# Kernel tuning notes

Measured on AMD Instinct MI355X. Metric: run time of the kernel, lower is better.

## Reference

```python
import jax, jax.numpy as jnp
import numpy as np

DILATIONS = (1, 2, 4, 8)
NUM_ITER = 10
W1 = 0.3
W2 = 0.01
# 3x3 neighborhood excluding center, row-major (matches get_kernel ordering)
OFFS = ((0, 0), (0, 1), (0, 2), (1, 0), (1, 2), (2, 0), (2, 1), (2, 2))
# distance weights: sqrt(2) for diagonals (indices 0,2,5,7), 1 otherwise
POS_VALS = np.array([np.sqrt(2), 1.0, np.sqrt(2), 1.0, 1.0, np.sqrt(2), 1.0, np.sqrt(2)], dtype=np.float32)


def dilated_neighbors(x):
    # x: [b, c, h, w] -> [b, c, K, h, w], K = 8 * len(DILATIONS)
    b, c, h, w = x.shape
    outs = []
    for d in DILATIONS:
        xp = jnp.pad(x, ((0, 0), (0, 0), (d, d), (d, d)), mode='edge')
        for di, dj in OFFS:
            outs.append(jax.lax.dynamic_slice(xp, (0, 0, di * d, dj * d), (b, c, h, w)))
    return jnp.stack(outs, axis=2)


def pos_vec():
    # [K] concatenation of POS_VALS * d for each dilation
    return jnp.concatenate([jnp.asarray(POS_VALS) * d for d in DILATIONS], axis=0)


def setup_inputs() -> dict:
    key = jax.random.key(0)
    k1, k2 = jax.random.split(key)
    imgs = jax.random.normal(k1, (8, 3, 128, 128), dtype=jnp.float32)
    masks = jax.random.uniform(k2, (8, 21, 128, 128), dtype=jnp.float32)
    return {"imgs": imgs, "masks": masks}


def reference(imgs, masks):
    # pixel affinity: [b, 1, K, h, w]
    nb = dilated_neighbors(imgs)                                  # [b,c,K,h,w]
    diff = jnp.abs(nb - imgs[:, :, None, :, :])
    std = jnp.std(nb, axis=2, ddof=1, keepdims=True)              # unbiased, like torch.std
    aff = -((diff / (std + 1e-8) / W1) ** 2).mean(axis=1, keepdims=True)

    # position affinity: constant over b,h,w -> compute on the [K] vector
    pos = pos_vec()                                               # [K]
    pos_std = jnp.std(pos, ddof=1)
    pos_aff = -((pos / (pos_std + 1e-8) / W1) ** 2)

    aff = jax.nn.softmax(aff, axis=2) + W2 * jax.nn.softmax(pos_aff)[None, None, :, None, None]

    for _ in range(NUM_ITER):
        masks = (dilated_neighbors(masks) * aff).sum(axis=2)
    return masks
```

## Files before the change

kernel.cpp:

```cpp
#include <hip/hip_runtime.h>
#include <cmath>

#define B_   8
#define CI_  3
#define CM_  21
#define H_   128
#define W_   128
#define K_   32
#define PAD_ 8
#define PW_  144
#define PH_  144
#define NC_  3

typedef float f4 __attribute__((ext_vector_type(4)));
typedef _Float16 h4 __attribute__((ext_vector_type(4)));
typedef _Float16 h8v __attribute__((ext_vector_type(8)));

struct PosSoft { float v[K_]; };

template<int S>
__device__ __forceinline__ h4 shwh(h4 A, h4 B) {
  return __builtin_shufflevector(A, B, S, S + 1, S + 2, S + 3);
}

__device__ __forceinline__ h4 lda(const _Float16* p, int off) {
  return *reinterpret_cast<const h4*>(p + off);
}

__global__ __launch_bounds__(128) void aff_kernel(const float* __restrict__ imgs,
                                                  _Float16* __restrict__ aff,
                                                  PosSoft ps) {
  constexpr int OI[8] = {-1,-1,-1, 0, 0, 1, 1, 1};
  constexpr int OJ[8] = {-1, 0, 1,-1, 1,-1, 0, 1};
  const int j = threadIdx.x;
  const int i = blockIdx.x;
  const int b = blockIdx.y;
  const float* img = imgs + (size_t)b * CI_ * H_ * W_;

  float ctr[CI_];
#pragma unroll
  for (int c = 0; c < CI_; ++c) ctr[c] = img[c * H_ * W_ + i * W_ + j];

  float s[CI_] = {0.f, 0.f, 0.f}, s2[CI_] = {0.f, 0.f, 0.f};
#pragma unroll
  for (int k = 0; k < K_; ++k) {
    const int d  = 1 << (k >> 3);
    const int ci = min(max(i + OI[k & 7] * d, 0), H_ - 1);
    const int cj = min(max(j + OJ[k & 7] * d, 0), W_ - 1);
#pragma unroll
    for (int c = 0; c < CI_; ++c) {
      float v = img[c * H_ * W_ + ci * W_ + cj];
      s[c] += v; s2[c] += v * v;
    }
  }

  float inv[CI_];
#pragma unroll
  for (int c = 0; c < CI_; ++c) {
    float mean = s[c] * (1.f / K_);
    float var  = (s2[c] - (float)K_ * mean * mean) * (1.f / (K_ - 1));
    var = fmaxf(var, 0.f);
    inv[c] = 1.f / ((sqrtf(var) + 1e-8f) * 0.3f);
  }

  float araw[K_];
#pragma unroll
  for (int k = 0; k < K_; ++k) {
    const int d  = 1 << (k >> 3);
    const int ci = min(max(i + OI[k & 7] * d, 0), H_ - 1);
    const int cj = min(max(j + OJ[k & 7] * d, 0), W_ - 1);
    float t = 0.f;
#pragma unroll
    for (int c = 0; c < CI_; ++c) {
      float v  = img[c * H_ * W_ + ci * W_ + cj];
      float dd = fabsf(v - ctr[c]) * inv[c];
      t += dd * dd;
    }
    araw[k] = -t * (1.f / CI_);
  }

  float m = araw[0];
#pragma unroll
  for (int k = 1; k < K_; ++k) m = fmaxf(m, araw[k]);
  float sum = 0.f;
#pragma unroll
  for (int k = 0; k < K_; ++k) { float e = __expf(araw[k] - m); araw[k] = e; sum += e; }
  const float rs = 1.f / sum;

  _Float16* ap = aff + ((size_t)(b * H_ + i) * K_) * W_ + j;
#pragma unroll
  for (int k = 0; k < K_; ++k) ap[k * W_] = (_Float16)(araw[k] * rs + ps.v[k]);
}

__global__ void pad_kernel(const float* __restrict__ src, _Float16* __restrict__ dst,
                           int total4) {
  int idx = blockIdx.x * blockDim.x + threadIdx.x;
  if (idx >= total4) return;
  int q  = idx % (PW_ / 4);
  int t  = idx / (PW_ / 4);
  int pi = t % PH_;
  int p  = t / PH_;
  int i = min(max(pi - PAD_, 0), H_ - 1);
  const float* srow = src + (size_t)p * (H_ * W_) + i * W_;
  h4 o;
#pragma unroll
  for (int e = 0; e < 4; ++e) {
    int j = min(max(q * 4 + e - PAD_, 0), W_ - 1);
    o[e] = (_Float16)srow[j];
  }
  *reinterpret_cast<h4*>(dst + (size_t)p * (PH_ * PW_) + pi * PW_ + q * 4) = o;
}

#define LX(C, DR, CO) (lb + ((C) * 2880 + ((DR) + 8) * 144 + ((CO) + 8)))
#define LDSH(IDX) (*reinterpret_cast<const h4*>(&sm[(IDX)]))

#define HCH(C, ACC) do {                                                       \
    h4 m2 = LDSH(LX(C, 0, -8)), m1 = LDSH(LX(C, 0, -4));                       \
    h4 c0 = LDSH(LX(C, 0, 0)),  c1 = LDSH(LX(C, 0, 4));                        \
    h4 c2 = LDSH(LX(C, 0, 8));                                                 \
    ACC += a03 * shwh<3>(m1, c0) + a04 * shwh<1>(c0, c1);                      \
    ACC += a13 * shwh<2>(m1, c0) + a14 * shwh<2>(c0, c1);                      \
    ACC += a23 * m1 + a24 * c1;                                                \
    ACC += a33 * m2 + a34 * c2;                                                \
  } while (0)

#define VCHS(D, SM, A0, A1, A2, A5, A6, A7, C, ACC) do {                       \
    h4 ua = LDSH(LX(C, -(D), -4)), ub = LDSH(LX(C, -(D), 0));                  \
    h4 uc = LDSH(LX(C, -(D), 4));                                              \
    ACC += A0 * shwh<SM>(ua, ub) + A1 * ub + A2 * shwh<D>(ub, uc);             \
    h4 da = LDSH(LX(C, (D), -4)), db = LDSH(LX(C, (D), 0));                    \
    h4 dc = LDSH(LX(C, (D), 4));                                               \
    ACC += A5 * shwh<SM>(da, db) + A6 * db + A7 * shwh<D>(db, dc);             \
  } while (0)

#define VCH4(A0, A1, A2, A5, A6, A7, C, ACC) do {                              \
    h4 ua = LDSH(LX(C, -4, -4)), ub = LDSH(LX(C, -4, 0)), uc = LDSH(LX(C, -4, 4)); \
    ACC += A0 * ua + A1 * ub + A2 * uc;                                        \
    h4 da = LDSH(LX(C, 4, -4)), db = LDSH(LX(C, 4, 0)), dc = LDSH(LX(C, 4, 4)); \
    ACC += A5 * da + A6 * db + A7 * dc;                                        \
  } while (0)

#define VCH8(A0, A1, A2, A5, A6, A7, C, ACC) do {                              \
    h4 ua = LDSH(LX(C, -8, -8)), ub = LDSH(LX(C, -8, 0)), uc = LDSH(LX(C, -8, 8)); \
    ACC += A0 * ua + A1 * ub + A2 * uc;                                        \
    h4 da = LDSH(LX(C, 8, -8)), db = LDSH(LX(C, 8, 0)), dc = LDSH(LX(C, 8, 8)); \
    ACC += A5 * da + A6 * db + A7 * dc;                                        \
  } while (0)

template <int PADOUT>
__global__ __launch_bounds__(128, 3) void iter_kernel(const _Float16* __restrict__ src,
                                                      const _Float16* __restrict__ aff,
                                                      void* __restrict__ dstv) {
  __shared__ _Float16 sm[NC_ * 20 * PW_];

  const int bid  = blockIdx.x;
  const int b    = bid & 7;
  const int t    = bid >> 3;
  const int grp  = t % 7;
  const int tile = t / 7;

  const int tid = threadIdx.x;
  const int qx  = tid & 31;
  const int j0  = qx * 4;
  const int tr  = tid >> 5;
  const int i   = tile * 4 + tr;
  const int i0  = tile * 4;
  const int c0  = grp * NC_;

  constexpr int CHP = PH_ * PW_;

  const _Float16* ab = aff + ((size_t)(b * H_ + i) * K_) * W_ + j0;
  h4 a00 = lda(ab,  0 * W_), a01 = lda(ab,  1 * W_), a02 = lda(ab,  2 * W_),
     a03 = lda(ab,  3 * W_), a04 = lda(ab,  4 * W_), a05 = lda(ab,  5 * W_),
     a06 = lda(ab,  6 * W_), a07 = lda(ab,  7 * W_);
  h4 a10 = lda(ab,  8 * W_), a11 = lda(ab,  9 * W_), a12 = lda(ab, 10 * W_),
     a13 = lda(ab, 11 * W_), a14 = lda(ab, 12 * W_), a15 = lda(ab, 13 * W_),
     a16 = lda(ab, 14 * W_), a17 = lda(ab, 15 * W_);
  h4 a20 = lda(ab, 16 * W_), a21 = lda(ab, 17 * W_), a22 = lda(ab, 18 * W_),
     a23 = lda(ab, 19 * W_), a24 = lda(ab, 20 * W_), a25 = lda(ab, 21 * W_),
     a26 = lda(ab, 22 * W_), a27 = lda(ab, 23 * W_);
  h4 a30 = lda(ab, 24 * W_), a31 = lda(ab, 25 * W_), a32 = lda(ab, 26 * W_),
     a33 = lda(ab, 27 * W_), a34 = lda(ab, 28 * W_), a35 = lda(ab, 29 * W_),
     a36 = lda(ab, 30 * W_), a37 = lda(ab, 31 * W_);

  {
    const _Float16* pl = src + (size_t)(b * CM_ + c0) * CHP + (size_t)i0 * PW_;
    for (int s = tid; s < 1080; s += 128) {
      int c = s / 360;
      int r = s - c * 360;
      h8v v = *reinterpret_cast<const h8v*>(pl + (size_t)c * CHP + r * 8);
      *reinterpret_cast<h8v*>(&sm[c * 2880 + r * 8]) = v;
    }
  }
  __syncthreads();

  const int lb = tr * PW_ + j0;

  h4 acc0 = (h4){0, 0, 0, 0};
  h4 acc1 = (h4){0, 0, 0, 0};
  h4 acc2 = (h4){0, 0, 0, 0};

  HCH(0, acc0); HCH(1, acc1); HCH(2, acc2);

  VCHS(1, 3, a00, a01, a02, a05, a06, a07, 0, acc0);
  VCHS(1, 3, a00, a01, a02, a05, a06, a07, 1, acc1);
  VCHS(1, 3, a00, a01, a02, a05, a06, a07, 2, acc2);

  VCHS(2, 2, a10, a11, a12, a15, a16, a17, 0, acc0);
  VCHS(2, 2, a10, a11, a12, a15, a16, a17, 1, acc1);
  VCHS(2, 2, a10, a11, a12, a15, a16, a17, 2, acc2);

  VCH4(a20, a21, a22, a25, a26, a27, 0, acc0);
  VCH4(a20, a21, a22, a25, a26, a27, 1, acc1);
  VCH4(a20, a21, a22, a25, a26, a27, 2, acc2);

  VCH8(a30, a31, a32, a35, a36, a37, 0, acc0);
  VCH8(a30, a31, a32, a35, a36, a37, 1, acc1);
  VCH8(a30, a31, a32, a35, a36, a37, 2, acc2);

  if (PADOUT) {
    _Float16* d0 = (_Float16*)dstv + (size_t)(b * CM_ + c0) * CHP;
    _Float16* d1 = d0 + CHP;
    _Float16* d2 = d0 + 2 * CHP;
    const int pr = i + PAD_;
    const int r0 = (i == 0)      ? 0         : pr;
    const int r1 = (i == H_ - 1) ? (PH_ - 1) : pr;
    for (int r = r0; r <= r1; ++r) {
      _Float16* row0 = d0 + r * PW_;
      _Float16* row1 = d1 + r * PW_;
      _Float16* row2 = d2 + r * PW_;
      *reinterpret_cast<h4*>(row0 + PAD_ + j0) = acc0;
      *reinterpret_cast<h4*>(row1 + PAD_ + j0) = acc1;
      *reinterpret_cast<h4*>(row2 + PAD_ + j0) = acc2;
      if (qx == 0) {
        h4 s0 = (h4){acc0.x, acc0.x, acc0.x, acc0.x};
        h4 s1 = (h4){acc1.x, acc1.x, acc1.x, acc1.x};
        h4 s2 = (h4){acc2.x, acc2.x, acc2.x, acc2.x};
        *reinterpret_cast<h4*>(row0) = s0; *reinterpret_cast<h4*>(row0 + 4) = s0;
        *reinterpret_cast<h4*>(row1) = s1; *reinterpret_cast<h4*>(row1 + 4) = s1;
        *reinterpret_cast<h4*>(row2) = s2; *reinterpret_cast<h4*>(row2 + 4) = s2;
      }
      if (qx == 31) {
        h4 s0 = (h4){acc0.w, acc0.w, acc0.w, acc0.w};
        h4 s1 = (h4){acc1.w, acc1.w, acc1.w, acc1.w};
        h4 s2 = (h4){acc2.w, acc2.w, acc2.w, acc2.w};
        *reinterpret_cast<h4*>(row0 + PW_ - 8) = s0; *reinterpret_cast<h4*>(row0 + PW_ - 4) = s0;
        *reinterpret_cast<h4*>(row1 + PW_ - 8) = s1; *reinterpret_cast<h4*>(row1 + PW_ - 4) = s1;
        *reinterpret_cast<h4*>(row2 + PW_ - 8) = s2; *reinterpret_cast<h4*>(row2 + PW_ - 4) = s2;
      }
    }
  } else {
    float* dc = (float*)dstv + (size_t)(b * CM_ + c0) * (H_ * W_) + (size_t)i * W_ + j0;
    *reinterpret_cast<f4*>(dc)                 = __builtin_convertvector(acc0, f4);
    *reinterpret_cast<f4*>(dc + (H_ * W_))     = __builtin_convertvector(acc1, f4);
    *reinterpret_cast<f4*>(dc + 2 * (H_ * W_)) = __builtin_convertvector(acc2, f4);
  }
}

extern "C" void kernel_launch(void* const* d_in, const int* in_sizes, int n_in,
                              void* d_out, int out_size, void* d_ws, size_t ws_size,
                              hipStream_t stream) {
  const float* imgs  = (const float*)d_in[0];
  const float* masks = (const float*)d_in[1];
  float* out = (float*)d_out;

  char* ws = (char*)d_ws;
  const size_t affBytes = (size_t)B_ * K_ * H_ * W_ * sizeof(_Float16);
  const size_t padBytes = (size_t)B_ * CM_ * PH_ * PW_ * sizeof(_Float16);
  _Float16* aff = (_Float16*)ws;
  _Float16* P0  = (_Float16*)(ws + affBytes);
  _Float16* P1  = (_Float16*)(ws + affBytes + padBytes);

  PosSoft ps;
  {
    const double pv[8] = {1.4142135623730951, 1.0, 1.4142135623730951, 1.0,
                          1.0, 1.4142135623730951, 1.0, 1.4142135623730951};
    double pos[K_];
    for (int di = 0; di < 4; ++di) {
      double d = (double)(1 << di);
      for (int o = 0; o < 8; ++o) pos[di * 8 + o] = pv[o] * d;
    }
    double mean = 0; for (int k = 0; k < K_; ++k) mean += pos[k]; mean /= K_;
    double var = 0;  for (int k = 0; k < K_; ++k) { double dd = pos[k] - mean; var += dd * dd; }
    var /= (K_ - 1);
    double sd = sqrt(var);
    double pa[K_]; double m = -1e300;
    for (int k = 0; k < K_; ++k) {
      double r = pos[k] / ((sd + 1e-8) * 0.3);
      pa[k] = -(r * r);
      if (pa[k] > m) m = pa[k];
    }
    double es = 0; for (int k = 0; k < K_; ++k) { pa[k] = exp(pa[k] - m); es += pa[k]; }
    for (int k = 0; k < K_; ++k) ps.v[k] = (float)(0.01 * pa[k] / es);
  }

  aff_kernel<<<dim3(H_, B_), 128, 0, stream>>>(imgs, aff, ps);

  const int total4 = B_ * CM_ * PH_ * (PW_ / 4);
  pad_kernel<<<(total4 + 255) / 256, 256, 0, stream>>>(masks, P0, total4);

  const int nblk = B_ * 7 * (H_ / 4);
  _Float16* s = P0;
  _Float16* d = P1;
  for (int it = 0; it < 9; ++it) {
    iter_kernel<1><<<nblk, 128, 0, stream>>>(s, aff, (void*)d);
    _Float16* tm = s; s = d; d = tm;
  }
  iter_kernel<0><<<nblk, 128, 0, stream>>>(s, aff, (void*)out);
}
```

Measured before the change: 132.2 us.

## Stage aff image rows in LDS and enlarge iter tile with direct dilation-8 loads

The affinity kernel now stages a 17-row band of the three image channels in shared memory, so the 32-neighbour gathers read LDS instead of global memory. The iteration kernel doubles its tile to 8 rows with 256 threads and keeps only a 16-row halo in LDS. The dilation-8 taps, which fall outside that halo, are loaded straight from global memory into registers. This reduces redundant halo loads per output row, at the cost of more register pressure and more uncoalesced-ish global loads.

```diff
diff --git a/kernel.cpp b/kernel.cpp
--- a/kernel.cpp
+++ b/kernel.cpp
@@ -11,6 +11,8 @@
 #define PW_  144
 #define PH_  144
 #define NC_  3
+#define TR_  8
+#define SR_  16
 
 typedef float f4 __attribute__((ext_vector_type(4)));
 typedef _Float16 h4 __attribute__((ext_vector_type(4)));
@@ -30,6 +32,8 @@
 __global__ __launch_bounds__(128) void aff_kernel(const float* __restrict__ imgs,
                                                   _Float16* __restrict__ aff,
                                                   PosSoft ps) {
+  __shared__ float sim[CI_ * 17 * W_];
+
   constexpr int OI[8] = {-1,-1,-1, 0, 0, 1, 1, 1};
   constexpr int OJ[8] = {-1, 0, 1,-1, 1,-1, 0, 1};
   const int j = threadIdx.x;
@@ -37,19 +41,30 @@
   const int b = blockIdx.y;
   const float* img = imgs + (size_t)b * CI_ * H_ * W_;
 
+  for (int L = threadIdx.x; L < CI_ * 17 * (W_ / 4); L += 128) {
+    int c   = L / (17 * 32);
+    int rem = L - c * (17 * 32);
+    int s   = rem >> 5;
+    int q   = rem & 31;
+    int r   = min(max(i - 8 + s, 0), H_ - 1);
+    f4 v = *reinterpret_cast<const f4*>(&img[(size_t)c * (H_ * W_) + r * W_ + q * 4]);
+    *reinterpret_cast<f4*>(&sim[c * (17 * W_) + s * W_ + q * 4]) = v;
+  }
+  __syncthreads();
+
   float ctr[CI_];
 #pragma unroll
-  for (int c = 0; c < CI_; ++c) ctr[c] = img[c * H_ * W_ + i * W_ + j];
+  for (int c = 0; c < CI_; ++c) ctr[c] = sim[c * (17 * W_) + 8 * W_ + j];
 
   float s[CI_] = {0.f, 0.f, 0.f}, s2[CI_] = {0.f, 0.f, 0.f};
 #pragma unroll
   for (int k = 0; k < K_; ++k) {
     const int d  = 1 << (k >> 3);
-    const int ci = min(max(i + OI[k & 7] * d, 0), H_ - 1);
+    const int rs = 8 + OI[k & 7] * d;
     const int cj = min(max(j + OJ[k & 7] * d, 0), W_ - 1);
 #pragma unroll
     for (int c = 0; c < CI_; ++c) {
-      float v = img[c * H_ * W_ + ci * W_ + cj];
+      float v = sim[c * (17 * W_) + rs * W_ + cj];
       s[c] += v; s2[c] += v * v;
     }
   }
@@ -67,12 +82,12 @@
 #pragma unroll
   for (int k = 0; k < K_; ++k) {
     const int d  = 1 << (k >> 3);
-    const int ci = min(max(i + OI[k & 7] * d, 0), H_ - 1);
+    const int rs = 8 + OI[k & 7] * d;
     const int cj = min(max(j + OJ[k & 7] * d, 0), W_ - 1);
     float t = 0.f;
 #pragma unroll
     for (int c = 0; c < CI_; ++c) {
-      float v  = img[c * H_ * W_ + ci * W_ + cj];
+      float v  = sim[c * (17 * W_) + rs * W_ + cj];
       float dd = fabsf(v - ctr[c]) * inv[c];
       t += dd * dd;
     }
@@ -111,7 +126,7 @@
   *reinterpret_cast<h4*>(dst + (size_t)p * (PH_ * PW_) + pi * PW_ + q * 4) = o;
 }
 
-#define LX(C, DR, CO) (lb + ((C) * 2880 + ((DR) + 8) * 144 + ((CO) + 8)))
+#define LX(C, DR, CO) (lb + ((C) * (SR_ * PW_) + ((DR) + 4) * PW_ + ((CO) + 8)))
 #define LDSH(IDX) (*reinterpret_cast<const h4*>(&sm[(IDX)]))
 
 #define HCH(C, ACC) do {                                                       \
@@ -140,18 +155,11 @@
     ACC += A5 * da + A6 * db + A7 * dc;                                        \
   } while (0)
 
-#define VCH8(A0, A1, A2, A5, A6, A7, C, ACC) do {                              \
-    h4 ua = LDSH(LX(C, -8, -8)), ub = LDSH(LX(C, -8, 0)), uc = LDSH(LX(C, -8, 8)); \
-    ACC += A0 * ua + A1 * ub + A2 * uc;                                        \
-    h4 da = LDSH(LX(C, 8, -8)), db = LDSH(LX(C, 8, 0)), dc = LDSH(LX(C, 8, 8)); \
-    ACC += A5 * da + A6 * db + A7 * dc;                                        \
-  } while (0)
-
 template <int PADOUT>
-__global__ __launch_bounds__(128, 3) void iter_kernel(const _Float16* __restrict__ src,
+__global__ __launch_bounds__(256, 3) void iter_kernel(const _Float16* __restrict__ src,
                                                       const _Float16* __restrict__ aff,
                                                       void* __restrict__ dstv) {
-  __shared__ _Float16 sm[NC_ * 20 * PW_];
+  __shared__ _Float16 sm[NC_ * SR_ * PW_];
 
   const int bid  = blockIdx.x;
   const int b    = bid & 7;
@@ -163,8 +171,8 @@
   const int qx  = tid & 31;
   const int j0  = qx * 4;
   const int tr  = tid >> 5;
-  const int i   = tile * 4 + tr;
-  const int i0  = tile * 4;
+  const int i   = tile * TR_ + tr;
+  const int i0  = tile * TR_;
   const int c0  = grp * NC_;
 
   constexpr int CHP = PH_ * PW_;
@@ -183,13 +191,23 @@
      a33 = lda(ab, 27 * W_), a34 = lda(ab, 28 * W_), a35 = lda(ab, 29 * W_),
      a36 = lda(ab, 30 * W_), a37 = lda(ab, 31 * W_);
 
+  const _Float16* g0 = src + (size_t)(b * CM_ + c0) * CHP + (i + PAD_) * PW_ + (j0 + PAD_);
+  const _Float16* g1 = g0 + CHP;
+  const _Float16* g2 = g0 + 2 * CHP;
+  h4 u80 = lda(g0, -8 * PW_ - 8), u81 = lda(g0, -8 * PW_), u82 = lda(g0, -8 * PW_ + 8);
+  h4 d80 = lda(g0,  8 * PW_ - 8), d81 = lda(g0,  8 * PW_), d82 = lda(g0,  8 * PW_ + 8);
+  h4 u90 = lda(g1, -8 * PW_ - 8), u91 = lda(g1, -8 * PW_), u92 = lda(g1, -8 * PW_ + 8);
+  h4 d90 = lda(g1,  8 * PW_ - 8), d91 = lda(g1,  8 * PW_), d92 = lda(g1,  8 * PW_ + 8);
+  h4 uA0 = lda(g2, -8 * PW_ - 8), uA1 = lda(g2, -8 * PW_), uA2 = lda(g2, -8 * PW_ + 8);
+  h4 dA0 = lda(g2,  8 * PW_ - 8), dA1 = lda(g2,  8 * PW_), dA2 = lda(g2,  8 * PW_ + 8);
+
   {
-    const _Float16* pl = src + (size_t)(b * CM_ + c0) * CHP + (size_t)i0 * PW_;
-    for (int s = tid; s < 1080; s += 128) {
-      int c = s / 360;
-      int r = s - c * 360;
+    const _Float16* pl = src + (size_t)(b * CM_ + c0) * CHP + (size_t)(i0 + 4) * PW_;
+    for (int s = tid; s < NC_ * (SR_ * PW_ / 8); s += 256) {
+      int c = s / (SR_ * PW_ / 8);
+      int r = s - c * (SR_ * PW_ / 8);
       h8v v = *reinterpret_cast<const h8v*>(pl + (size_t)c * CHP + r * 8);
-      *reinterpret_cast<h8v*>(&sm[c * 2880 + r * 8]) = v;
+      *reinterpret_cast<h8v*>(&sm[c * (SR_ * PW_) + r * 8]) = v;
     }
   }
   __syncthreads();
@@ -214,9 +232,12 @@
   VCH4(a20, a21, a22, a25, a26, a27, 1, acc1);
   VCH4(a20, a21, a22, a25, a26, a27, 2, acc2);
 
-  VCH8(a30, a31, a32, a35, a36, a37, 0, acc0);
-  VCH8(a30, a31, a32, a35, a36, a37, 1, acc1);
-  VCH8(a30, a31, a32, a35, a36, a37, 2, acc2);
+  acc0 += a30 * u80 + a31 * u81 + a32 * u82;
+  acc0 += a35 * d80 + a36 * d81 + a37 * d82;
+  acc1 += a30 * u90 + a31 * u91 + a32 * u92;
+  acc1 += a35 * d90 + a36 * d91 + a37 * d92;
+  acc2 += a30 * uA0 + a31 * uA1 + a32 * uA2;
+  acc2 += a35 * dA0 + a36 * dA1 + a37 * dA2;
 
   if (PADOUT) {
     _Float16* d0 = (_Float16*)dstv + (size_t)(b * CM_ + c0) * CHP;
@@ -299,12 +320,12 @@
   const int total4 = B_ * CM_ * PH_ * (PW_ / 4);
   pad_kernel<<<(total4 + 255) / 256, 256, 0, stream>>>(masks, P0, total4);
 
-  const int nblk = B_ * 7 * (H_ / 4);
+  const int nblk = B_ * 7 * (H_ / TR_);
   _Float16* s = P0;
   _Float16* d = P1;
   for (int it = 0; it < 9; ++it) {
-    iter_kernel<1><<<nblk, 128, 0, stream>>>(s, aff, (void*)d);
+    iter_kernel<1><<<nblk, 256, 0, stream>>>(s, aff, (void*)d);
     _Float16* tm = s; s = d; d = tm;
   }
-  iter_kernel<0><<<nblk, 128, 0, stream>>>(s, aff, (void*)out);
-}
+  iter_kernel<0><<<nblk, 256, 0, stream>>>(s, aff, (void*)out);
+}
```

Result: slower. 146.3 us (+10.6%).
